# Performance work log

Measured on AMD Instinct MI355X. Metric: run time of the kernel, lower is better.

## Reference

```python
import jax, jax.numpy as jnp
import numpy as np

B, S, D = 2, 2048, 4096
N_HEADS, N_KV_HEADS, HEAD_DIM = 32, 8, 128
Q_DIM = N_HEADS * HEAD_DIM        # 4096
KV_DIM = N_KV_HEADS * HEAD_DIM    # 1024
N_REP = N_HEADS // N_KV_HEADS
ROPE_THETA = 500000.0


def make_freqs_cis(seqlen, head_dim, theta):
    # Interleaved (sin, cos) pairs per rotary frequency, matching the module's
    # einsum/flip RoPE convention: row1 = x0*sin + x1*cos, row0 = x0*cos - x1*sin.
    inv_freq = 1.0 / (theta ** (np.arange(0, head_dim, 2, dtype=np.float32) / head_dim))
    t = np.arange(seqlen, dtype=np.float32)
    ang = np.outer(t, inv_freq)                       # [S, hd/2]
    fc = np.stack([np.sin(ang), np.cos(ang)], axis=-1)  # [S, hd/2, 2]
    return jnp.asarray(fc.reshape(seqlen, head_dim))


def apply_rotary_emb(xq, xk, freqs_cis):
    # xq: [B,S,Hq,hd], xk: [B,S,Hkv,hd], freqs_cis: [S,hd]
    xq_shape, xk_shape = xq.shape, xk.shape
    xq2 = xq.reshape(*xq.shape[:-1], -1, 2)
    xk2 = xk.reshape(*xk.shape[:-1], -1, 2)
    fc = freqs_cis.reshape(freqs_cis.shape[0], 1, -1, 2)   # [S,1,hd/2,2]
    # row_1 = <x, fc>
    xq_row1 = jnp.einsum('bshpi,shpi->bshp', xq2, fc)
    xk_row1 = jnp.einsum('bshpi,shpi->bshp', xk2, fc)
    # flipped fc with negated second component: (f1, -f0)
    fc_flip = jnp.flip(fc, axis=-1) * jnp.array([1.0, -1.0], dtype=fc.dtype)
    xq_row0 = jnp.einsum('bshpi,shpi->bshp', xq2, fc_flip)
    xk_row0 = jnp.einsum('bshpi,shpi->bshp', xk2, fc_flip)
    xq_out = jnp.stack([xq_row0, xq_row1], axis=-1).reshape(xq_shape)
    xk_out = jnp.stack([xk_row0, xk_row1], axis=-1).reshape(xk_shape)
    return xq_out, xk_out


def setup_inputs() -> dict:
    key = jax.random.key(0)
    k1, k2, k3 = jax.random.split(key, 3)
    x = jax.random.normal(k1, (B, S, D), dtype=jnp.float32)
    wqkv = jax.random.normal(k2, (D, Q_DIM + 2 * KV_DIM), dtype=jnp.float32) * 0.02
    wo = jax.random.normal(k3, (Q_DIM, D), dtype=jnp.float32) * 0.02
    freqs_cis = make_freqs_cis(S, HEAD_DIM, ROPE_THETA)
    return {"x": x, "freqs_cis": freqs_cis, "wqkv": wqkv, "wo": wo, "is_causal": 1}


def reference(x, freqs_cis, wqkv, wo, is_causal):
    bsz, seqlen, _ = x.shape
    xqkv = jnp.einsum('bsd,de->bse', x, wqkv)
    xq = xqkv[..., :Q_DIM].reshape(bsz, seqlen, N_HEADS, HEAD_DIM)
    xk = xqkv[..., Q_DIM:Q_DIM + KV_DIM].reshape(bsz, seqlen, N_KV_HEADS, HEAD_DIM)
    xv = xqkv[..., Q_DIM + KV_DIM:].reshape(bsz, seqlen, N_KV_HEADS, HEAD_DIM)
    xq, xk = apply_rotary_emb(xq, xk, freqs_cis)
    # [B,H,S,hd]
    xq = xq.transpose(0, 2, 1, 3)
    xk = jnp.repeat(xk.transpose(0, 2, 1, 3), N_REP, axis=1)
    xv = jnp.repeat(xv.transpose(0, 2, 1, 3), N_REP, axis=1)
    scale = 1.0 / jnp.sqrt(jnp.asarray(HEAD_DIM, dtype=xq.dtype))
    scores = jnp.einsum('bhqd,bhkd->bhqk', xq, xk) * scale
    if is_causal:
        mask = jnp.tril(jnp.ones((seqlen, seqlen), dtype=bool))
        scores = jnp.where(mask, scores, jnp.finfo(scores.dtype).min)
    attn = jax.nn.softmax(scores, axis=-1)
    out = jnp.einsum('bhqk,bhkd->bhqd', attn, xv)
    out = out.transpose(0, 2, 1, 3).reshape(bsz, seqlen, Q_DIM)
    return jnp.einsum('bsd,de->bse', out, wo)
```

## Files before the change

### kernel.cpp

```cpp
#include <hip/hip_runtime.h>
#include <stdint.h>
#include <stddef.h>

#define BB 2
#define SS 2048
#define DD 4096
#define NH 32
#define NKV 8
#define HD 128
#define QDIM 4096
#define KVDIM 1024
#define NQKV 6144
#define NTILES 64
#define QK_SCALE_L2E 0.12751744f

typedef __bf16 bf16;
typedef __bf16 bf16x8 __attribute__((ext_vector_type(8)));
typedef __bf16 bf16x4 __attribute__((ext_vector_type(4)));
typedef float f32x4 __attribute__((ext_vector_type(4)));

#define MFMA16(a, b, c) __builtin_amdgcn_mfma_f32_16x16x32_bf16((a), (b), (c), 0, 0, 0)
#define BAR() __builtin_amdgcn_s_barrier()
#define VMW10() asm volatile("s_waitcnt vmcnt(10)" ::: "memory")

typedef __attribute__((address_space(1))) void GASV;
typedef __attribute__((address_space(3))) void LASV;

__device__ __forceinline__ void gload_lds16(const void* g, void* l) {
    __builtin_amdgcn_global_load_lds((GASV*)g, (LASV*)l, 16, 0, 0);
}

__device__ __forceinline__ float fexp2(float x) {
    float r;
    asm("v_exp_f32 %0, %1" : "=v"(r) : "v"(x));
    return r;
}

__global__ __launch_bounds__(256) void k_cvt_x(const float* __restrict__ in,
                                               bf16* __restrict__ out) {
    size_t i = ((size_t)blockIdx.x * 256 + threadIdx.x) * 8;
    const float4 a = *(const float4*)(in + i);
    const float4 b = *(const float4*)(in + i + 4);
    bf16x8 v;
    v[0] = (bf16)a.x; v[1] = (bf16)a.y; v[2] = (bf16)a.z; v[3] = (bf16)a.w;
    v[4] = (bf16)b.x; v[5] = (bf16)b.y; v[6] = (bf16)b.z; v[7] = (bf16)b.w;
    *(bf16x8*)(out + i) = v;
}

__global__ __launch_bounds__(256) void k_tr_cvt(const float* __restrict__ in,
                                                bf16* __restrict__ out, int R, int C) {
    __shared__ float tile[64][65];
    const int t = threadIdx.x;
    const int tx = t & 15, ty = t >> 4;
    const int r0 = blockIdx.y * 64, c0 = blockIdx.x * 64;
#pragma unroll
    for (int p = 0; p < 4; ++p) {
        const float4 v = *(const float4*)(in + (size_t)(r0 + p * 16 + ty) * C + c0 + tx * 4);
        tile[p * 16 + ty][tx * 4 + 0] = v.x;
        tile[p * 16 + ty][tx * 4 + 1] = v.y;
        tile[p * 16 + ty][tx * 4 + 2] = v.z;
        tile[p * 16 + ty][tx * 4 + 3] = v.w;
    }
    __syncthreads();
#pragma unroll
    for (int p = 0; p < 4; ++p) {
        const int oc = c0 + p * 16 + ty;
        bf16x4 pk;
#pragma unroll
        for (int j = 0; j < 4; ++j) pk[j] = (bf16)tile[tx * 4 + j][p * 16 + ty];
        *(bf16x4*)(out + (size_t)oc * R + r0 + tx * 4) = pk;
    }
}


__device__ __forceinline__ void stage_half(char* ldsRegion, const bf16* gsrc) {
    const int t = threadIdx.x;
    const int wid = t >> 6;
#pragma unroll
    for (int i = 0; i < 2; ++i) {
        const int off = i * 8192 + t * 16;
        const int row = off >> 7;
        const int pc = (off >> 4) & 7;
        const int lc = pc ^ (row & 7);
        gload_lds16(gsrc + (size_t)row * 4096 + lc * 8,
                    ldsRegion + i * 8192 + wid * 1024);
    }
}

__device__ __forceinline__ void gemm256(const bf16* __restrict__ At,
                                        const bf16* __restrict__ Bt,
                                        char* LB, f32x4 acc[8][4]) {
    const int tid = threadIdx.x, lane = tid & 63, wid = tid >> 6;
    const int wm = wid >> 2, wn = wid & 3;
    const int l15 = lane & 15, l4 = lane >> 4;

    const f32x4 vz = {0.f, 0.f, 0.f, 0.f};
#pragma unroll
    for (int m = 0; m < 8; ++m)
#pragma unroll
        for (int n = 0; n < 4; ++n) acc[m][n] = vz;

    auto Areg = [&](int db, int h) -> char* { return LB + db * 32768 + h * 16384; };
    auto Breg = [&](int db, int h) -> char* { return LB + 65536 + db * 32768 + h * 16384; };

    bf16x8 Aa[2][4], Ab[2][4], B0r[2][2], B1r[2][2];

    auto loadA = [&](bf16x8 dst[2][4], int db, int h) {
        char* base = Areg(db, h);
#pragma unroll
        for (int kk = 0; kk < 2; ++kk)
#pragma unroll
            for (int mf = 0; mf < 4; ++mf) {
                const int row = wm * 64 + mf * 16 + l15;
                const int cc = kk * 4 + l4;
                dst[kk][mf] = *(const bf16x8*)(base + row * 128 + ((cc ^ (row & 7)) << 4));
            }
    };
    auto loadB = [&](bf16x8 dst[2][2], int db, int h) {
        char* base = Breg(db, h);
#pragma unroll
        for (int kk = 0; kk < 2; ++kk)
#pragma unroll
            for (int nf = 0; nf < 2; ++nf) {
                const int row = wn * 32 + nf * 16 + l15;
                const int cc = kk * 4 + l4;
                dst[kk][nf] = *(const bf16x8*)(base + row * 128 + ((cc ^ (row & 7)) << 4));
            }
    };
    auto stA = [&](int tau, int h) {
        stage_half(Areg(tau & 1, h), At + (size_t)(h * 128) * 4096 + tau * 64);
    };
    auto stB = [&](int tau, int h) {
        stage_half(Breg(tau & 1, h), Bt + (size_t)(h * 128) * 4096 + tau * 64);
    };
    auto mma = [&](bf16x8 A[2][4], bf16x8 B[2][2], int mb, int nb) {
        __builtin_amdgcn_s_setprio(1);
#pragma unroll
        for (int kk = 0; kk < 2; ++kk)
#pragma unroll
            for (int mf = 0; mf < 4; ++mf)
#pragma unroll
                for (int nf = 0; nf < 2; ++nf)
                    acc[mb + mf][nb + nf] = MFMA16(A[kk][mf], B[kk][nf], acc[mb + mf][nb + nf]);
        __builtin_amdgcn_s_setprio(0);
    };

    stA(0, 0); stB(0, 0); stB(0, 1); stA(0, 1);
    stA(1, 0); stB(1, 0); stB(1, 1); stA(1, 1);
    asm volatile("s_waitcnt vmcnt(8)" ::: "memory");
    BAR();
    loadA(Aa, 0, 0);
    loadB(B0r, 0, 0);

#pragma unroll 1
    for (int tau = 0; tau < NTILES - 2; ++tau) {
        const int db = tau & 1, ndb = db ^ 1;
        loadB(B1r, db, 1);
        stA(tau + 2, 0);
        VMW10(); BAR();
        mma(Aa, B0r, 0, 0);
        BAR();
        loadA(Ab, db, 1);
        stB(tau + 2, 0);
        VMW10(); BAR();
        mma(Aa, B1r, 0, 2);
        BAR();
        stB(tau + 2, 1);
        VMW10(); BAR();
        mma(Ab, B0r, 4, 0);
        BAR();
        loadA(Aa, ndb, 0);
        loadB(B0r, ndb, 0);
        stA(tau + 2, 1);
        VMW10(); BAR();
        mma(Ab, B1r, 4, 2);
        BAR();
    }

    asm volatile("s_waitcnt vmcnt(0)" ::: "memory");
    BAR();
#pragma unroll 1
    for (int tau = NTILES - 2; tau < NTILES; ++tau) {
        const int db = tau & 1, ndb = db ^ 1;
        loadB(B1r, db, 1);
        BAR(); mma(Aa, B0r, 0, 0); BAR();
        loadA(Ab, db, 1);
        BAR(); mma(Aa, B1r, 0, 2); BAR();
        BAR(); mma(Ab, B0r, 4, 0); BAR();
        if (tau < NTILES - 1) { loadA(Aa, ndb, 0); loadB(B0r, ndb, 0); }
        BAR(); mma(Ab, B1r, 4, 2); BAR();
    }
}

__global__ __launch_bounds__(512, 2) void k_gemm_qkv(const bf16* __restrict__ A,
                                                     const bf16* __restrict__ Bt,
                                                     const float* __restrict__ fc,
                                                     bf16* __restrict__ Qb,
                                                     bf16* __restrict__ Kb,
                                                     bf16* __restrict__ VTb) {
    __shared__ __align__(16) char LB[131072];
    f32x4 acc[8][4];
    const int bx = blockIdx.x, by = blockIdx.y;
    gemm256(A + (size_t)by * 256 * 4096, Bt + (size_t)bx * 256 * 4096, LB, acc);

    const int tid = threadIdx.x, lane = tid & 63, wid = tid >> 6;
    const int wm = wid >> 2, wn = wid & 3;
    const int l15 = lane & 15, l4 = lane >> 4;
    const int n0r = bx * 256;
#pragma unroll
    for (int mf = 0; mf < 8; ++mf) {
        const int rowbase = by * 256 + (mf >> 2) * 128 + wm * 64 + (mf & 3) * 16 + l4 * 4;
#pragma unroll
        for (int nf = 0; nf < 4; ++nf) {
            const int col = n0r + (nf >> 1) * 128 + wn * 32 + (nf & 1) * 16 + l15;
            f32x4 v = acc[mf][nf];
            if (n0r < QDIM + KVDIM) {
                const int d = col & (HD - 1);
                const int dp = d & ~1;
                const float sgn = (d & 1) ? 1.f : -1.f;
#pragma unroll
                for (int r = 0; r < 4; ++r) {
                    const int row = rowbase + r;
                    const int s = row & (SS - 1);
                    const float2 sc = *(const float2*)(fc + s * HD + dp);
                    const float partner = __shfl_xor(v[r], 1);
                    float res = v[r] * sc.y + sgn * partner * sc.x;
                    if (n0r < QDIM) {
                        res *= QK_SCALE_L2E;
                        Qb[(size_t)row * QDIM + col] = (bf16)res;
                    } else {
                        Kb[(size_t)row * KVDIM + (col - QDIM)] = (bf16)res;
                    }
                }
            } else {
                const int hdv = col - (QDIM + KVDIM);
                const int kvh = hdv >> 7, dd = hdv & (HD - 1);
                const int bb = rowbase >> 11, s = rowbase & (SS - 1);
                bf16x4 pk;
#pragma unroll
                for (int r = 0; r < 4; ++r) pk[r] = (bf16)v[r];
                *(bf16x4*)(VTb + ((size_t)((bb * NKV + kvh) * HD + dd)) * SS + s) = pk;
            }
        }
    }
}

__global__ __launch_bounds__(512, 2) void k_gemm_out(const bf16* __restrict__ A,
                                                     const bf16* __restrict__ Bt,
                                                     float* __restrict__ out) {
    __shared__ __align__(16) char LB[131072];
    f32x4 acc[8][4];
    const int bx = blockIdx.x, by = blockIdx.y;
    gemm256(A + (size_t)by * 256 * 4096, Bt + (size_t)bx * 256 * 4096, LB, acc);

    const int tid = threadIdx.x, lane = tid & 63, wid = tid >> 6;
    const int wm = wid >> 2, wn = wid & 3;
    const int l15 = lane & 15, l4 = lane >> 4;
#pragma unroll
    for (int mf = 0; mf < 8; ++mf) {
        const int row = by * 256 + (mf >> 2) * 128 + wm * 64 + (mf & 3) * 16 + l4 * 4;
#pragma unroll
        for (int nf = 0; nf < 4; ++nf) {
            const int col = bx * 256 + (nf >> 1) * 128 + wn * 32 + (nf & 1) * 16 + l15;
#pragma unroll
            for (int r = 0; r < 4; ++r) out[(size_t)(row + r) * DD + col] = acc[mf][nf][r];
        }
    }
}

__global__ __launch_bounds__(256, 2) void k_attn(const bf16* __restrict__ Qb,
                                                 const bf16* __restrict__ Kb,
                                                 const bf16* __restrict__ VTb,
                                                 bf16* __restrict__ Ob) {
    __shared__ __align__(16) bf16 Ks[64 * 128];
    __shared__ __align__(16) bf16 Vs[128 * 64];
    __shared__ __align__(16) bf16 Ps[4][32 * 88];
    const int jj = blockIdx.x, h = blockIdx.y, b = blockIdx.z;
    const int kvh = h >> 2;
    const int tid = threadIdx.x, lane = tid & 63, w = tid >> 6;
    const int l15 = lane & 15, l4 = lane >> 4;

    const bf16* Kg = Kb + (size_t)b * SS * KVDIM + kvh * HD;
    const bf16* Vg = VTb + (size_t)(b * NKV + kvh) * HD * SS;

    int4 kreg[4], vreg[4];
    const f32x4 vz = {0.f, 0.f, 0.f, 0.f};

    auto issue_kv = [&](int t) {
#pragma unroll
        for (int i = 0; i < 4; ++i) {
            const int off = i * 4096 + tid * 16;
            const int row = off >> 8;
            const int cc = (off >> 4) & 15;
            kreg[i] = *(const int4*)((const char*)(Kg + (size_t)(t * 64 + row) * KVDIM) + cc * 16);
        }
#pragma unroll
        for (int i = 0; i < 4; ++i) {
            const int off = i * 4096 + tid * 16;
            const int row = off >> 7;
            const int cc = (off >> 4) & 7;
            vreg[i] = *(const int4*)((const char*)(Vg + (size_t)row * SS + t * 64) + cc * 16);
        }
    };

#pragma unroll 1
    for (int pj = 0; pj < 2; ++pj) {
        const int j = pj ? (15 - jj) : jj;
        const int q0 = j * 128;
        const int nt = 2 * j + 2;

        bf16x8 qf[2][4];
#pragma unroll
        for (int m = 0; m < 2; ++m) {
            const int qrow = q0 + w * 32 + m * 16 + l15;
            const bf16* qb = Qb + ((size_t)(b * SS + qrow) << 12) + h * HD + l4 * 8;
#pragma unroll
            for (int kc = 0; kc < 4; ++kc) qf[m][kc] = *(const bf16x8*)(qb + kc * 32);
        }

        f32x4 o[2][8];
#pragma unroll
        for (int m = 0; m < 2; ++m)
#pragma unroll
            for (int df = 0; df < 8; ++df) o[m][df] = vz;
        float m_run[2][4], l_run[2][4];
#pragma unroll
        for (int m = 0; m < 2; ++m)
#pragma unroll
            for (int r = 0; r < 4; ++r) { m_run[m][r] = -1e30f; l_run[m][r] = 0.f; }

        issue_kv(0);

        for (int t = 0; t < nt; ++t) {
            __syncthreads();
#pragma unroll
            for (int i = 0; i < 4; ++i) {
                const int off = i * 4096 + tid * 16;
                const int row = off >> 8;
                const int cc = (off >> 4) & 15;
                const int lc = cc ^ (row & 7);
                *(int4*)((char*)Ks + row * 256 + lc * 16) = kreg[i];
            }
#pragma unroll
            for (int i = 0; i < 4; ++i) {
                const int off = i * 4096 + tid * 16;
                const int row = off >> 7;
                const int cc = (off >> 4) & 7;
                const int lc = cc ^ (row & 7);
                *(int4*)((char*)Vs + row * 128 + lc * 16) = vreg[i];
            }
            __syncthreads();

            if (t + 1 < nt) issue_kv(t + 1);

            f32x4 sa[2][4];
#pragma unroll
            for (int m = 0; m < 2; ++m)
#pragma unroll
                for (int n = 0; n < 4; ++n) sa[m][n] = vz;
            __builtin_amdgcn_s_setprio(1);
#pragma unroll
            for (int kc = 0; kc < 4; ++kc)
#pragma unroll
                for (int n = 0; n < 4; ++n) {
                    const int krow = n * 16 + l15;
                    const int cc = kc * 4 + l4;
                    const bf16x8 kf =
                        *(const bf16x8*)((const char*)Ks + (krow << 8) + ((cc ^ (krow & 7)) << 4));
                    sa[0][n] = MFMA16(qf[0][kc], kf, sa[0][n]);
                    sa[1][n] = MFMA16(qf[1][kc], kf, sa[1][n]);
                }
            __builtin_amdgcn_s_setprio(0);

            if (t >= 2 * j) {
#pragma unroll
                for (int m = 0; m < 2; ++m)
#pragma unroll
                    for (int n = 0; n < 4; ++n)
#pragma unroll
                        for (int r = 0; r < 4; ++r) {
                            const int col = t * 64 + n * 16 + l15;
                            const int qr = q0 + w * 32 + m * 16 + l4 * 4 + r;
                            if (col > qr) sa[m][n][r] = -1e30f;
                        }
            }

#pragma unroll
            for (int m = 0; m < 2; ++m)
#pragma unroll
                for (int r = 0; r < 4; ++r) {
                    float mx = fmaxf(fmaxf(sa[m][0][r], sa[m][1][r]),
                                     fmaxf(sa[m][2][r], sa[m][3][r]));
#pragma unroll
                    for (int mk = 1; mk <= 8; mk <<= 1) mx = fmaxf(mx, __shfl_xor(mx, mk));
                    const float mn = fmaxf(m_run[m][r], mx);
                    const float alpha = fexp2(m_run[m][r] - mn);
                    m_run[m][r] = mn;
                    float rs = 0.f;
#pragma unroll
                    for (int n = 0; n < 4; ++n) {
                        const float p = fexp2(sa[m][n][r] - mn);
                        sa[m][n][r] = p;
                        rs += p;
                    }
#pragma unroll
                    for (int mk = 1; mk <= 8; mk <<= 1) rs += __shfl_xor(rs, mk);
                    l_run[m][r] = l_run[m][r] * alpha + rs;
#pragma unroll
                    for (int df = 0; df < 8; ++df) o[m][df][r] *= alpha;
                }

#pragma unroll
            for (int m = 0; m < 2; ++m)
#pragma unroll
                for (int n = 0; n < 4; ++n)
#pragma unroll
                    for (int r = 0; r < 4; ++r)
                        Ps[w][(m * 16 + l4 * 4 + r) * 88 + n * 16 + l15] = (bf16)sa[m][n][r];

            bf16x8 pf0[2], pf1[2];
#pragma unroll
            for (int ks = 0; ks < 2; ++ks) {
                pf0[ks] = *(const bf16x8*)(&Ps[w][l15 * 88 + ks * 32 + l4 * 8]);
                pf1[ks] = *(const bf16x8*)(&Ps[w][(16 + l15) * 88 + ks * 32 + l4 * 8]);
            }

            __builtin_amdgcn_s_setprio(1);
#pragma unroll
            for (int df = 0; df < 8; ++df)
#pragma unroll
                for (int ks = 0; ks < 2; ++ks) {
                    const int vrow = df * 16 + l15;
                    const int cc = ks * 4 + l4;
                    const bf16x8 vf =
                        *(const bf16x8*)((const char*)Vs + (vrow << 7) + ((cc ^ (vrow & 7)) << 4));
                    o[0][df] = MFMA16(pf0[ks], vf, o[0][df]);
                    o[1][df] = MFMA16(pf1[ks], vf, o[1][df]);
                }
            __builtin_amdgcn_s_setprio(0);
        }

#pragma unroll
        for (int m = 0; m < 2; ++m)
#pragma unroll
            for (int r = 0; r < 4; ++r) {
                const float inv = 1.f / l_run[m][r];
                const size_t row = (size_t)(b * SS + q0 + w * 32 + m * 16 + l4 * 4 + r);
#pragma unroll
                for (int df = 0; df < 8; ++df)
                    Ob[(row << 12) + h * HD + df * 16 + l15] = (bf16)(o[m][df][r] * inv);
            }
    }
}

extern "C" void kernel_launch(void* const* d_in, const int* in_sizes, int n_in,
                              void* d_out, int out_size, void* d_ws, size_t ws_size,
                              hipStream_t stream) {
    const float* x    = (const float*)d_in[0];
    const float* fc   = (const float*)d_in[1];
    const float* wqkv = (const float*)d_in[2];
    const float* wo   = (const float*)d_in[3];

    char* wsp = (char*)d_ws;
    const size_t MB = (size_t)1 << 20;
    bf16* xb    = (bf16*)(wsp);
    bf16* wqkvT = (bf16*)(wsp + 32 * MB);
    bf16* woT   = (bf16*)(wsp + 32 * MB);
    bf16* Qb    = (bf16*)(wsp + 80 * MB);
    bf16* Kb    = (bf16*)(wsp + 112 * MB);
    bf16* VTb   = (bf16*)(wsp + 120 * MB);
    bf16* Ab    = (bf16*)(wsp);
    float* out  = (float*)d_out;

    k_cvt_x<<<8192, 256, 0, stream>>>(x, xb);
    k_tr_cvt<<<dim3(NQKV / 64, DD / 64), 256, 0, stream>>>(wqkv, wqkvT, DD, NQKV);
    k_gemm_qkv<<<dim3(NQKV / 256, (BB * SS) / 256), 512, 0, stream>>>(xb, wqkvT, fc, Qb, Kb, VTb);
    k_tr_cvt<<<dim3(DD / 64, QDIM / 64), 256, 0, stream>>>(wo, woT, QDIM, DD);
    k_attn<<<dim3(8, NH, BB), 256, 0, stream>>>(Qb, Kb, VTb, Ab);
    k_gemm_out<<<dim3(DD / 256, (BB * SS) / 256), 512, 0, stream>>>(Ab, woT, out);
}
```

Measured before the change: 608.8 us.

## Add XCD-aware block swizzle and relax GEMM pipeline waits

Remaps block indices in both GEMM kernels and the attention kernel so that neighbouring tiles land on the same XCD, aiming for better L2 reuse of the shared A/B panels and K/V. The GEMM main loop also drops two of its vmcnt waits and changes another to vmcnt(8). The two-iteration tail loses all of its barriers. The weaker waiting risks reading LDS before the staged data has arrived, since the waits now rely on the ordering of earlier loads.

```diff
diff --git a/kernel.cpp b/kernel.cpp
--- a/kernel.cpp
+++ b/kernel.cpp
@@ -22,6 +22,7 @@
 #define MFMA16(a, b, c) __builtin_amdgcn_mfma_f32_16x16x32_bf16((a), (b), (c), 0, 0, 0)
 #define BAR() __builtin_amdgcn_s_barrier()
 #define VMW10() asm volatile("s_waitcnt vmcnt(10)" ::: "memory")
+#define VMW8() asm volatile("s_waitcnt vmcnt(8)" ::: "memory")
 
 typedef __attribute__((address_space(1))) void GASV;
 typedef __attribute__((address_space(3))) void LASV;
@@ -103,7 +104,7 @@
     auto Areg = [&](int db, int h) -> char* { return LB + db * 32768 + h * 16384; };
     auto Breg = [&](int db, int h) -> char* { return LB + 65536 + db * 32768 + h * 16384; };
 
-    bf16x8 Aa[2][4], Ab[2][4], B0r[2][2], B1r[2][2];
+    bf16x8 RA[2][4], RAb[2][4], RB0[2][2], RB1[2][2];
 
     auto loadA = [&](bf16x8 dst[2][4], int db, int h) {
         char* base = Areg(db, h);
@@ -147,33 +148,34 @@
 
     stA(0, 0); stB(0, 0); stB(0, 1); stA(0, 1);
     stA(1, 0); stB(1, 0); stB(1, 1); stA(1, 1);
-    asm volatile("s_waitcnt vmcnt(8)" ::: "memory");
+    VMW8();
     BAR();
-    loadA(Aa, 0, 0);
-    loadB(B0r, 0, 0);
+    loadA(RA, 0, 0); loadB(RB0, 0, 0);
 
 #pragma unroll 1
     for (int tau = 0; tau < NTILES - 2; ++tau) {
         const int db = tau & 1, ndb = db ^ 1;
-        loadB(B1r, db, 1);
+        loadB(RB1, db, 1);
         stA(tau + 2, 0);
-        VMW10(); BAR();
-        mma(Aa, B0r, 0, 0);
-        BAR();
-        loadA(Ab, db, 1);
+        BAR();
+        mma(RA, RB0, 0, 0);
+        BAR();
+        loadA(RAb, db, 1);
         stB(tau + 2, 0);
-        VMW10(); BAR();
-        mma(Aa, B1r, 0, 2);
+        BAR();
+        mma(RA, RB1, 0, 2);
         BAR();
         stB(tau + 2, 1);
-        VMW10(); BAR();
-        mma(Ab, B0r, 4, 0);
-        BAR();
-        loadA(Aa, ndb, 0);
-        loadB(B0r, ndb, 0);
+        VMW10();
+        BAR();
+        mma(RAb, RB0, 4, 0);
+        BAR();
+        loadA(RA, ndb, 0);
+        loadB(RB0, ndb, 0);
         stA(tau + 2, 1);
-        VMW10(); BAR();
-        mma(Ab, B1r, 4, 2);
+        VMW8();
+        BAR();
+        mma(RAb, RB1, 4, 2);
         BAR();
     }
 
@@ -182,14 +184,22 @@
 #pragma unroll 1
     for (int tau = NTILES - 2; tau < NTILES; ++tau) {
         const int db = tau & 1, ndb = db ^ 1;
-        loadB(B1r, db, 1);
-        BAR(); mma(Aa, B0r, 0, 0); BAR();
-        loadA(Ab, db, 1);
-        BAR(); mma(Aa, B1r, 0, 2); BAR();
-        BAR(); mma(Ab, B0r, 4, 0); BAR();
-        if (tau < NTILES - 1) { loadA(Aa, ndb, 0); loadB(B0r, ndb, 0); }
-        BAR(); mma(Ab, B1r, 4, 2); BAR();
-    }
+        loadB(RB1, db, 1);
+        mma(RA, RB0, 0, 0);
+        loadA(RAb, db, 1);
+        mma(RA, RB1, 0, 2);
+        mma(RAb, RB0, 4, 0);
+        if (tau < NTILES - 1) { loadA(RA, ndb, 0); loadB(RB0, ndb, 0); }
+        mma(RAb, RB1, 4, 2);
+    }
+}
+
+__device__ __forceinline__ void xcd_swizzle(int gx, int& bx, int& by) {
+    const int nwg = gx * gridDim.y;
+    int lin = by * gx + bx;
+    lin = (lin & 7) * (nwg >> 3) + (lin >> 3);
+    bx = lin % gx;
+    by = lin / gx;
 }
 
 __global__ __launch_bounds__(512, 2) void k_gemm_qkv(const bf16* __restrict__ A,
@@ -200,7 +210,8 @@
                                                      bf16* __restrict__ VTb) {
     __shared__ __align__(16) char LB[131072];
     f32x4 acc[8][4];
-    const int bx = blockIdx.x, by = blockIdx.y;
+    int bx = blockIdx.x, by = blockIdx.y;
+    xcd_swizzle(NQKV / 256, bx, by);
     gemm256(A + (size_t)by * 256 * 4096, Bt + (size_t)bx * 256 * 4096, LB, acc);
 
     const int tid = threadIdx.x, lane = tid & 63, wid = tid >> 6;
@@ -250,7 +261,8 @@
                                                      float* __restrict__ out) {
     __shared__ __align__(16) char LB[131072];
     f32x4 acc[8][4];
-    const int bx = blockIdx.x, by = blockIdx.y;
+    int bx = blockIdx.x, by = blockIdx.y;
+    xcd_swizzle(DD / 256, bx, by);
     gemm256(A + (size_t)by * 256 * 4096, Bt + (size_t)bx * 256 * 4096, LB, acc);
 
     const int tid = threadIdx.x, lane = tid & 63, wid = tid >> 6;
@@ -275,7 +287,9 @@
     __shared__ __align__(16) bf16 Ks[64 * 128];
     __shared__ __align__(16) bf16 Vs[128 * 64];
     __shared__ __align__(16) bf16 Ps[4][32 * 88];
-    const int jj = blockIdx.x, h = blockIdx.y, b = blockIdx.z;
+    int lin = (blockIdx.z * NH + blockIdx.y) * 8 + blockIdx.x;
+    lin = (lin & 7) * 64 + (lin >> 3);
+    const int jj = lin & 7, h = (lin >> 3) & (NH - 1), b = lin >> 8;
     const int kvh = h >> 2;
     const int tid = threadIdx.x, lane = tid & 63, w = tid >> 6;
     const int l15 = lane & 15, l4 = lane >> 4;
```

Measured after the change: 605.3 us. Within noise of the previous version (-0.6%).
